# Kernel tuning notes

Measured on AMD Instinct MI355X. Metric: run time of the kernel, lower is better.

## Reference

```python
import jax, jax.numpy as jnp
import numpy as np

INF = 1e8
EPS = 1e-6
STRIDES = (8, 16, 32, 64, 128)
FEAT_SIZES = ((100, 128), (50, 64), (25, 32), (13, 16), (7, 8))
NUM_CLASSES = 81  # args.num_classes + 1
BG = NUM_CLASSES
TOPK1, TOPK2 = 3, 1
RATIO = 0.9
FRACTION = 0.5
B, G = 16, 32
NPER = [h * w for h, w in FEAT_SIZES]
OFFS = np.cumsum([0] + NPER)


def gen_trf():
    j = [2 ** i for i in range(8)]
    r1 = 1 + 6 * j[0]; r2 = r1 + 2 * j[1]
    p2 = r2 + 2 * j[2] * 3; r3 = p2 + 2 * j[2]
    p3 = r3 + 2 * j[3] * 3; r4 = p3 + 2 * j[3]
    p4 = r4 + 2 * j[4] * 5; r5 = p4 + 2 * j[4]
    p5 = r5 + 2 * j[5] * 2
    p6 = p5 + 2 * j[6]; p7 = p6 + 2 * j[7]
    return [p2, p3, p4, p5, p6, p7]


def make_points_rfields():
    trfs = gen_trf()
    pts, rfs = [], []
    for lvl, (h, w) in enumerate(FEAT_SIZES):
        s = STRIDES[lvl]
        xs = jnp.arange(w, dtype=jnp.float32) * s + s // 2
        ys = jnp.arange(h, dtype=jnp.float32) * s + s // 2
        Y, X = jnp.meshgrid(ys, xs, indexing='ij')
        p = jnp.stack([X.reshape(-1), Y.reshape(-1)], -1)
        pts.append(p)
        rf = trfs[lvl + 1] * FRACTION  # fpn_layer == 'p3' -> rfnum = lvl + 1
        rfs.append(jnp.concatenate([p - rf / 2, p + rf / 2], -1))
    return jnp.concatenate(pts, 0), jnp.concatenate(rfs, 0)


def kl_overlaps(gts, anc):
    # BboxDistanceMetric mode='kl': Gaussian KL divergence -> 1/(1+kl); (G, N)
    c1 = (gts[:, :2] + gts[:, 2:]) / 2
    c2 = (anc[:, :2] + anc[:, 2:]) / 2
    w1 = gts[:, 2] - gts[:, 0] + EPS; h1 = gts[:, 3] - gts[:, 1] + EPS
    w2 = anc[:, 2] - anc[:, 0] + EPS; h2 = anc[:, 3] - anc[:, 1] + EPS
    dx = c1[:, None, 0] - c2[None, :, 0]; dy = c1[:, None, 1] - c2[None, :, 1]
    w1s = (w1 ** 2)[:, None]; h1s = (h1 ** 2)[:, None]
    w2s = (w2 ** 2)[None, :]; h2s = (h2 ** 2)[None, :]
    kl = (w2s / w1s + h2s / h1s + 4 * dx ** 2 / w1s + 4 * dy ** 2 / h1s
          + jnp.log(w1s / w2s) + jnp.log(h1s / h2s) - 2) / 2
    return 1.0 / (1.0 + kl)


def hie_assign(rf1, rf2, gts):
    ov1 = kl_overlaps(gts, rf1)
    ov2 = kl_overlaps(gts, rf2)
    N = rf1.shape[0]; Gn = gts.shape[0]
    max_ov = ov1.max(0)
    assigned = jnp.where((max_ov >= 0) & (max_ov < 0.8), 0, -1).astype(jnp.int32)
    gt_ids = jnp.arange(1, Gn + 1, dtype=jnp.int32)
    _, i1 = jax.lax.top_k(ov1, TOPK1)  # (G, k1)
    s1 = jnp.full((N,), -1, jnp.int32).at[i1.reshape(-1)].max(jnp.repeat(gt_ids, TOPK1))
    assigned = jnp.where(s1 > 0, s1, assigned)
    _, i2 = jax.lax.top_k(ov2, TOPK2)  # (G, k2) second hierarchy overrides
    s2 = jnp.full((N,), -1, jnp.int32).at[i2.reshape(-1)].max(jnp.repeat(gt_ids, TOPK2))
    return jnp.where(s2 > 0, s2, assigned)


def target_single(gts, glabels, points, rf1, rf2):
    Gn = gts.shape[0]
    assigned = hie_assign(rf1, rf2, gts)  # (N,) 1-based gt index, 0/-1 = bg
    areas = (gts[:, 2] - gts[:, 0]) * (gts[:, 3] - gts[:, 1])
    mask = (assigned - 1)[:, None] == jnp.arange(Gn)[None, :]
    am = jnp.where(mask, areas[None, :], INF)
    min_area = am.min(1); mi = jnp.argmin(am, 1)
    lab = jnp.where(min_area >= INF, BG, glabels[mi])
    g = gts[mi]
    bt = jnp.stack([points[:, 0] - g[:, 0], points[:, 1] - g[:, 1],
                    g[:, 2] - points[:, 0], g[:, 3] - points[:, 1]], -1)
    return lab, bt


def diou_loss(pred, tgt):
    lt = jnp.maximum(pred[:, :2], tgt[:, :2])
    rb = jnp.minimum(pred[:, 2:], tgt[:, 2:])
    wh = jnp.clip(rb - lt, 0.0)
    ov = wh[:, 0] * wh[:, 1]
    ap = (pred[:, 2] - pred[:, 0]) * (pred[:, 3] - pred[:, 1])
    ag = (tgt[:, 2] - tgt[:, 0]) * (tgt[:, 3] - tgt[:, 1])
    ious = ov / (ap + ag - ov + EPS)
    elt = jnp.minimum(pred[:, :2], tgt[:, :2])
    erb = jnp.maximum(pred[:, 2:], tgt[:, 2:])
    ewh = jnp.clip(erb - elt, 0.0)
    c2 = ewh[:, 0] ** 2 + ewh[:, 1] ** 2 + EPS
    rho2 = ((pred[:, 0] + pred[:, 2] - tgt[:, 0] - tgt[:, 2]) ** 2
            + (pred[:, 1] + pred[:, 3] - tgt[:, 1] - tgt[:, 3]) ** 2) / 4
    return 1.0 - (ious - rho2 / c2)


def _forward(cls_l, bbox_l, ctr_l, gt_bboxes, gt_labels):
    points, rf1 = make_points_rfields()
    c = (rf1[:, :2] + rf1[:, 2:]) / 2
    wh = (rf1[:, 2:] - rf1[:, :2]) * RATIO
    rf2 = jnp.concatenate([c - wh / 2, c + wh / 2], -1)
    labels_all, targets_all = jax.vmap(target_single, (0, 0, None, None, None))(
        gt_bboxes, gt_labels, points, rf1, rf2)
    labels_all = jax.lax.stop_gradient(labels_all)
    targets_all = jax.lax.stop_gradient(targets_all)
    # flatten level-major, image-minor (matches torch.cat order in loss)
    fc = jnp.concatenate([t.transpose(0, 2, 3, 1).reshape(-1, NUM_CLASSES) for t in cls_l], 0)
    fb = jnp.concatenate([t.transpose(0, 2, 3, 1).reshape(-1, 4) for t in bbox_l], 0)
    fo = jnp.concatenate([t.transpose(0, 2, 3, 1).reshape(-1) for t in ctr_l], 0)
    fl = jnp.concatenate([labels_all[:, OFFS[i]:OFFS[i + 1]].reshape(-1) for i in range(5)], 0)
    ft = jnp.concatenate([targets_all[:, OFFS[i]:OFFS[i + 1]].reshape(-1, 4) for i in range(5)], 0)
    fp = jnp.concatenate([jnp.tile(points[OFFS[i]:OFFS[i + 1]], (B, 1)) for i in range(5)], 0)
    pos = fl < BG
    posf = pos.astype(fc.dtype)
    num_pos = jnp.maximum(posf.sum(), 1.0)
    # sigmoid focal loss (alpha=0.25, gamma=2); bg label -> all-zero one-hot
    tgt = jax.nn.one_hot(fl, NUM_CLASSES, dtype=fc.dtype)
    p = jax.nn.sigmoid(fc)
    pt = (1 - p) * tgt + p * (1 - tgt)
    fw = (0.25 * tgt + 0.75 * (1 - tgt)) * pt ** 2
    bce = jnp.maximum(fc, 0) - fc * tgt + jnp.log1p(jnp.exp(-jnp.abs(fc)))
    loss_cls = (bce * fw).sum() / num_pos
    # centerness target (sanitized on negatives to avoid nan)
    bt = jnp.where(pos[:, None], ft, 1.0)
    lr_min = jnp.minimum(bt[:, 0], bt[:, 2]); lr_max = jnp.maximum(bt[:, 0], bt[:, 2])
    tb_min = jnp.minimum(bt[:, 1], bt[:, 3]); tb_max = jnp.maximum(bt[:, 1], bt[:, 3])
    ctr_tgt = jnp.sqrt(jnp.clip((lr_min / lr_max) * (tb_min / tb_max), 0.0)) * posf
    denom = jnp.maximum(ctr_tgt.sum(), 1e-6)
    # decode distances to boxes and DIoU loss weighted by centerness
    x, y = fp[:, 0], fp[:, 1]
    pb = jnp.stack([x - fb[:, 0], y - fb[:, 1], x + fb[:, 2], y + fb[:, 3]], -1)
    tb_box = jnp.stack([x - bt[:, 0], y - bt[:, 1], x + bt[:, 2], y + bt[:, 3]], -1)
    loss_bbox = (diou_loss(pb, tb_box) * ctr_tgt).sum() / denom
    # centerness BCE-with-logits, averaged by num_pos
    bce_c = jnp.maximum(fo, 0) - fo * ctr_tgt + jnp.log1p(jnp.exp(-jnp.abs(fo)))
    loss_ctr = (bce_c * posf).sum() / num_pos
    return jnp.stack([loss_cls, loss_bbox, loss_ctr])


def setup_inputs() -> dict:
    key = jax.random.key(0)
    ks = jax.random.split(key, 24)
    cls_l = [jax.random.normal(ks[i], (B, NUM_CLASSES, h, w), jnp.float32) - 4.0
             for i, (h, w) in enumerate(FEAT_SIZES)]
    bbox_l = [jax.random.uniform(ks[5 + i], (B, 4, h, w), jnp.float32) * 64.0 + 1.0
              for i, (h, w) in enumerate(FEAT_SIZES)]
    ctr_l = [jax.random.normal(ks[10 + i], (B, 1, h, w), jnp.float32)
             for i, (h, w) in enumerate(FEAT_SIZES)]
    cx = jax.random.uniform(ks[15], (B, G)) * 1000.0 + 12.0
    cy = jax.random.uniform(ks[16], (B, G)) * 776.0 + 12.0
    w = jax.random.uniform(ks[17], (B, G)) * 240.0 + 8.0
    h = jax.random.uniform(ks[18], (B, G)) * 240.0 + 8.0
    gt_bboxes = jnp.stack([cx - w / 2, cy - h / 2, cx + w / 2, cy + h / 2], -1)
    gt_labels = jax.random.randint(ks[19], (B, G), 0, 80)
    d = {}
    for i in range(5):
        d[f'cls{i}'] = cls_l[i]; d[f'bbox{i}'] = bbox_l[i]; d[f'ctr{i}'] = ctr_l[i]
    d['gt_bboxes'] = gt_bboxes
    d['gt_labels'] = gt_labels
    return d


def reference(cls0, cls1, cls2, cls3, cls4, bbox0, bbox1, bbox2, bbox3, bbox4,
              ctr0, ctr1, ctr2, ctr3, ctr4, gt_bboxes, gt_labels):
    return _forward([cls0, cls1, cls2, cls3, cls4],
                    [bbox0, bbox1, bbox2, bbox3, bbox4],
                    [ctr0, ctr1, ctr2, ctr3, ctr4], gt_bboxes, gt_labels)
```

## Files before the change

### kernel.cpp

```cpp
#include <hip/hip_runtime.h>
#include <math.h>
#include <limits.h>

#pragma clang fp contract(off)

#define N_ANCH 17064
#define BATCH  16
#define NGT    32
#define EPSF   1e-6f

#define NPB     512
#define NSTREAM 2048
#define L2E 1.44269504088896340736f
#define LN2 0.69314718055994530942f

#define C1   4147200
#define C2   5184000
#define C3   5443200
#define C4   5510592
#define TOT4 5528736

#define CTR_IMG 0
#define CTR_SUB 16
#define CTR_GLB 32

__device__ __forceinline__ float fexp2(float x){ return __builtin_amdgcn_exp2f(x); }
__device__ __forceinline__ float flog2(float x){ return __builtin_amdgcn_logf(x); }
__device__ __forceinline__ float frcp (float x){ return __builtin_amdgcn_rcpf(x); }

__device__ __forceinline__ void astore_u32(unsigned int* p, unsigned int v) {
  __hip_atomic_store(p, v, __ATOMIC_RELAXED, __HIP_MEMORY_SCOPE_AGENT);
}
__device__ __forceinline__ unsigned int aload_u32(const unsigned int* p) {
  return __hip_atomic_load(p, __ATOMIC_RELAXED, __HIP_MEMORY_SCOPE_AGENT);
}
__device__ __forceinline__ void astore_u64(unsigned long long* p, unsigned long long v) {
  __hip_atomic_store(p, v, __ATOMIC_RELAXED, __HIP_MEMORY_SCOPE_AGENT);
}
__device__ __forceinline__ unsigned long long aload_u64(const unsigned long long* p) {
  return __hip_atomic_load(p, __ATOMIC_RELAXED, __HIP_MEMORY_SCOPE_AGENT);
}
#define VMCNT0() asm volatile("s_waitcnt vmcnt(0)" ::: "memory")

struct Geo { int lvl; int j; int HW; float px; float py; };

__device__ __forceinline__ Geo geom(int n) {
  Geo g;
  if (n < 12800)      { g.lvl=0; g.j=n;       g.HW=12800; g.px=(float)((g.j & 127)*8 + 4);   g.py=(float)((g.j >> 7)*8 + 4);   }
  else if (n < 16000) { g.lvl=1; g.j=n-12800; g.HW=3200;  g.px=(float)((g.j & 63)*16 + 8);   g.py=(float)((g.j >> 6)*16 + 8);  }
  else if (n < 16800) { g.lvl=2; g.j=n-16000; g.HW=800;   g.px=(float)((g.j & 31)*32 + 16);  g.py=(float)((g.j >> 5)*32 + 16); }
  else if (n < 17008) { g.lvl=3; g.j=n-16800; g.HW=208;   g.px=(float)((g.j & 15)*64 + 32);  g.py=(float)((g.j >> 4)*64 + 32); }
  else                { g.lvl=4; g.j=n-17008; g.HW=56;    g.px=(float)((g.j & 7)*128 + 64);  g.py=(float)((g.j >> 3)*128 + 64);}
  return g;
}

__device__ __forceinline__ bool bet(float av, int ai, float bv, int bi) {
  return (av < bv) || (av == bv && ai < bi);
}

__device__ __forceinline__ void insert3min(float* v, int* i, float nv, int ni) {
  if (nv < v[0])      { v[2]=v[1]; i[2]=i[1]; v[1]=v[0]; i[1]=i[0]; v[0]=nv; i[0]=ni; }
  else if (nv < v[1]) { v[2]=v[1]; i[2]=i[1]; v[1]=nv; i[1]=ni; }
  else                { v[2]=nv; i[2]=ni; }
}

__device__ __forceinline__ void insert3tie(float* v, int* i, float nv, int ni) {
  if (!bet(nv, ni, v[2], i[2])) return;
  if (bet(nv, ni, v[0], i[0]))      { v[2]=v[1]; i[2]=i[1]; v[1]=v[0]; i[1]=i[0]; v[0]=nv; i[0]=ni; }
  else if (bet(nv, ni, v[1], i[1])) { v[2]=v[1]; i[2]=i[1]; v[1]=nv; i[1]=ni; }
  else                              { v[2]=nv; i[2]=ni; }
}

__device__ __forceinline__ float negterm(float x) {
  float ax = fabsf(x);
  float e  = fexp2(ax * -L2E);
  float r  = frcp(1.0f + e);
  float p  = (x >= 0.0f) ? r : e * r;
  float sp = fmaxf(x, 0.0f) + flog2(1.0f + e) * LN2;
  return 0.75f * (p * p) * sp;
}

__global__ void zeroK(int* __restrict__ ctr) {
  int i = threadIdx.x;
  if (i < 33) ctr[i] = 0;
}

__device__ __forceinline__ void final_combine(const unsigned long long* __restrict__ bpart,
                                              const unsigned long long* __restrict__ gsum,
                                              float* __restrict__ out,
                                              double* R, int t) {
  if (t < 16) {
    R[t]      = __longlong_as_double(aload_u64(&gsum[t]));
    R[16+t]   = __longlong_as_double(aload_u64(&bpart[t*5+0]));
    R[32+t]   = __longlong_as_double(aload_u64(&bpart[t*5+1]));
    R[48+t]   = __longlong_as_double(aload_u64(&bpart[t*5+2]));
    R[64+t]   = __longlong_as_double(aload_u64(&bpart[t*5+3]));
    R[80+t]   = __longlong_as_double(aload_u64(&bpart[t*5+4]));
  }
  __syncthreads();
  if (t == 0) {
    double sc = 0.0, sp = 0.0, sct = 0.0, sdi = 0.0, scb = 0.0;
    for (int i = 0; i < 16; ++i) sc += R[i];
    for (int i = 0; i < 16; ++i) {
      sc  += R[16+i];
      sp  += R[32+i];
      sct += R[48+i];
      sdi += R[64+i];
      scb += R[80+i];
    }
    double np_ = sp > 1.0 ? sp : 1.0;
    double dn  = sct > 1e-6 ? sct : 1e-6;
    out[0] = (float)(sc / np_);
    out[1] = (float)(sdi / dn);
    out[2] = (float)(scb / np_);
  }
}

__global__ __launch_bounds__(256) void fusedK(
    const float4* __restrict__ gtb, const int* __restrict__ glab,
    const float* __restrict__ c0, const float* __restrict__ c1, const float* __restrict__ c2,
    const float* __restrict__ c3, const float* __restrict__ c4,
    const float* __restrict__ bb0, const float* __restrict__ bb1, const float* __restrict__ bb2,
    const float* __restrict__ bb3, const float* __restrict__ bb4,
    const float* __restrict__ ct0, const float* __restrict__ ct1, const float* __restrict__ ct2,
    const float* __restrict__ ct3, const float* __restrict__ ct4,
    unsigned int* __restrict__ win, unsigned int* __restrict__ part,
    unsigned long long* __restrict__ bpart, unsigned long long* __restrict__ gsum,
    int* __restrict__ ctr, float* __restrict__ out) {
  __shared__ float sv[768];
  __shared__ int   si[768];
  __shared__ float tv[256];
  __shared__ int   ti[256];
  __shared__ float sh[256];
  __shared__ unsigned int ukeys[128];
  __shared__ double r0[256], r1[256], r2[256], r3[256], r4[256];
  __shared__ int sflag, sflag2;

  int t  = threadIdx.x;
  int bi = blockIdx.x;

  if (bi >= NPB) {
    int sb = bi - NPB;
    float local = 0.0f;
    for (int i = sb * 256 + t; i < TOT4; i += NSTREAM * 256) {
      const float4* p; int off;
      if (i < C1)      { p = (const float4*)c0; off = i; }
      else if (i < C2) { p = (const float4*)c1; off = i - C1; }
      else if (i < C3) { p = (const float4*)c2; off = i - C2; }
      else if (i < C4) { p = (const float4*)c3; off = i - C3; }
      else             { p = (const float4*)c4; off = i - C4; }
      float4 f = p[off];
      local += negterm(f.x);
      local += negterm(f.y);
      local += negterm(f.z);
      local += negterm(f.w);
    }
    sh[t] = local;
    __syncthreads();
    #pragma unroll
    for (int off = 128; off > 0; off >>= 1) {
      if (t < off) sh[t] += sh[t + off];
      __syncthreads();
    }
    if (t == 0) {
      astore_u32(&part[sb], __float_as_uint(sh[0]));
      VMCNT0();
      int old = atomicAdd(&ctr[CTR_SUB + (sb & 15)], 1);
      sflag = (old == 127);
    }
    __syncthreads();
    if (!sflag) return;

    int g = sb & 15;
    double v = 0.0;
    if (t < 128) v = (double)__uint_as_float(aload_u32(&part[g + (t << 4)]));
    r0[t] = v;
    __syncthreads();
    #pragma unroll
    for (int off = 128; off > 0; off >>= 1) {
      if (t < off) r0[t] += r0[t + off];
      __syncthreads();
    }
    if (t == 0) {
      astore_u64(&gsum[g], (unsigned long long)__double_as_longlong(r0[0]));
      VMCNT0();
      int old2 = atomicAdd(&ctr[CTR_GLB], 1);
      sflag2 = (old2 == 31);
    }
    __syncthreads();
    if (sflag2) final_combine(bpart, gsum, out, r0, t);
    return;
  }

  int blk = bi;
  int b = blk >> 5, g = blk & 31;
  {
    float4 GB = gtb[b * NGT + g];
    float c1x = (GB.x + GB.z) * 0.5f, c1y = (GB.y + GB.w) * 0.5f;
    float w1 = GB.z - GB.x + EPSF, h1 = GB.w - GB.y + EPSF;
    float w1s = w1 * w1, h1s = h1 * h1;
    float iw = 1.0f / w1s, ih = 1.0f / h1s;
    float iws = iw + ih;
    float Lg = logf(w1s) + logf(h1s);
    float Ay = 4.0f * ih;
    float Axc = 4.0f * iw;

    float v1[3] = {INFINITY, INFINITY, INFINITY};
    int   i1[3] = {INT_MAX, INT_MAX, INT_MAX};
    float v2 = INFINITY; int i2 = INT_MAX;

    #define DO_LEVEL(BASE, LGW, H, STRIDE, RF) do {                             \
      const int W_ = 1 << (LGW);                                                \
      float w2a = (RF) + 1e-6f;          float w2sa = w2a * w2a;                \
      float w2b = (RF) * 0.9f + 1e-6f;   float w2sb = w2b * w2b;                \
      float K1 = w2sa * iws + Lg - 2.0f * logf(w2sa) - 2.0f;                    \
      float K2 = w2sb * iws + Lg - 2.0f * logf(w2sb) - 2.0f;                    \
      int col = t & (W_ - 1);                                                   \
      float px = (float)(col * (STRIDE) + (STRIDE) / 2);                        \
      float dx = c1x - px;                                                      \
      float kx1 = Axc * dx * dx + K1;                                           \
      float kx2 = Axc * dx * dx + K2;                                           \
      int rstep = 256 >> (LGW);                                                 \
      for (int row = t >> (LGW); row < (H); row += rstep) {                     \
        float py = (float)(row * (STRIDE) + (STRIDE) / 2);                      \
        float dy = c1y - py;                                                    \
        float dy2 = dy * dy;                                                    \
        float k1 = fmaf(Ay, dy2, kx1);                                          \
        float k2 = fmaf(Ay, dy2, kx2);                                          \
        int n = (BASE) + (row << (LGW)) + col;                                  \
        if (k1 < v1[2]) insert3min(v1, i1, k1, n);                              \
        if (k2 < v2) { v2 = k2; i2 = n; }                                       \
      }                                                                         \
    } while (0)

    DO_LEVEL(0,     7, 100,   8,  45.5f);
    DO_LEVEL(12800, 6,  50,  16, 133.5f);
    DO_LEVEL(16000, 5,  25,  32, 213.5f);
    DO_LEVEL(16800, 4,  13,  64, 277.5f);
    DO_LEVEL(17008, 3,   7, 128, 405.5f);
    #undef DO_LEVEL

    sv[t*3+0] = v1[0]; sv[t*3+1] = v1[1]; sv[t*3+2] = v1[2];
    si[t*3+0] = i1[0]; si[t*3+1] = i1[1]; si[t*3+2] = i1[2];
    tv[t] = v2; ti[t] = i2;
    __syncthreads();
    for (int off = 128; off > 0; off >>= 1) {
      if (t < off) {
        #pragma unroll
        for (int k = 0; k < 3; ++k)
          insert3tie(&sv[t * 3], &si[t * 3], sv[(t + off) * 3 + k], si[(t + off) * 3 + k]);
        if (bet(tv[t + off], ti[t + off], tv[t], ti[t])) { tv[t] = tv[t + off]; ti[t] = ti[t + off]; }
      }
      __syncthreads();
    }
    if (t == 0) {
      astore_u32(&win[blk * 4 + 0], (unsigned int)si[0]);
      astore_u32(&win[blk * 4 + 1], (unsigned int)si[1]);
      astore_u32(&win[blk * 4 + 2], (unsigned int)si[2]);
      astore_u32(&win[blk * 4 + 3], (unsigned int)ti[0]);
      VMCNT0();
      int old = atomicAdd(&ctr[CTR_IMG + b], 1);
      sflag = (old == 31);
    }
    __syncthreads();
  }
  if (!sflag) return;

  if (t < 128) {
    int gg = t >> 2, s = t & 3;
    unsigned int n = aload_u32(&win[b * 128 + gg * 4 + s]);
    unsigned int pri = ((s == 3) ? 32u : 0u) + (unsigned int)gg;
    ukeys[t] = (n << 6) | pri;
  }
  __syncthreads();

  double a_cls = 0.0, a_pos = 0.0, a_ctr = 0.0, a_diou = 0.0, a_cbce = 0.0;

  if (t < 128) {
    unsigned int me = ukeys[t];
    unsigned int nn = me >> 6;
    bool alive = true;
    #pragma unroll 8
    for (int j = 0; j < 128; ++j) {
      unsigned int o = ukeys[j];
      if ((o >> 6) == nn && o > me) alive = false;
    }
    if (alive) {
      int n = (int)nn;
      int gg = (int)(me & 31u);
      int lab = glab[b * NGT + gg];
      float4 gb = gtb[b * NGT + gg];
      Geo G = geom(n);

      const float* bb; const float* ct; const float* cp;
      if (G.lvl == 0)      { bb = bb0; ct = ct0; cp = c0; }
      else if (G.lvl == 1) { bb = bb1; ct = ct1; cp = c1; }
      else if (G.lvl == 2) { bb = bb2; ct = ct2; cp = c2; }
      else if (G.lvl == 3) { bb = bb3; ct = ct3; cp = c3; }
      else                 { bb = bb4; ct = ct4; cp = c4; }

      const float* bp = bb + b * 4 * G.HW + G.j;
      float f0 = bp[0];
      float f1 = bp[G.HW];
      float f2 = bp[2 * G.HW];
      float f3 = bp[3 * G.HW];
      float fo = ct[b * G.HW + G.j];
      float xc = cp[((size_t)(b * 81 + lab)) * G.HW + G.j];

      {
        float ax = fabsf(xc);
        float e  = fexp2(ax * -L2E);
        float r  = frcp(1.0f + e);
        float p  = (xc >= 0.0f) ? r : e * r;
        float sp = fmaxf(xc, 0.0f) + flog2(1.0f + e) * LN2;
        float neg = 0.75f * (p * p) * sp;
        float omp = 1.0f - p;
        float pos = 0.25f * (omp * omp) * (sp - xc);
        a_cls += (double)(pos - neg);
      }

      float tx = G.px - gb.x, ty = G.py - gb.y, tz = gb.z - G.px, tw = gb.w - G.py;

      float lr_min = fminf(tx, tz), lr_max = fmaxf(tx, tz);
      float tb_min = fminf(ty, tw), tb_max = fmaxf(ty, tw);
      float prod = (lr_min / lr_max) * (tb_min / tb_max);
      float ctrt = sqrtf(fmaxf(prod, 0.0f));

      float pb0 = G.px - f0, pb1 = G.py - f1, pb2 = G.px + f2, pb3 = G.py + f3;
      float tb0 = G.px - tx, tb1 = G.py - ty, tb2 = G.px + tz, tb3 = G.py + tw;

      float ltx = fmaxf(pb0, tb0), lty = fmaxf(pb1, tb1);
      float rbx = fminf(pb2, tb2), rby = fminf(pb3, tb3);
      float whx = fmaxf(rbx - ltx, 0.0f), why = fmaxf(rby - lty, 0.0f);
      float ovl = whx * why;
      float ap = (pb2 - pb0) * (pb3 - pb1);
      float ag = (tb2 - tb0) * (tb3 - tb1);
      float ious = ovl / (ap + ag - ovl + EPSF);
      float eltx = fminf(pb0, tb0), elty = fminf(pb1, tb1);
      float erbx = fmaxf(pb2, tb2), erby = fmaxf(pb3, tb3);
      float ewx = fmaxf(erbx - eltx, 0.0f), ewy = fmaxf(erby - elty, 0.0f);
      float c2v = ewx * ewx + ewy * ewy + EPSF;
      float sx = pb0 + pb2 - tb0 - tb2;
      float sy = pb1 + pb3 - tb1 - tb3;
      float rho2 = (sx * sx + sy * sy) * 0.25f;
      float dl = 1.0f - (ious - rho2 / c2v);

      a_pos  += 1.0;
      a_ctr  += (double)ctrt;
      a_diou += (double)(dl * ctrt);
      a_cbce += (double)(fmaxf(fo, 0.0f) - fo * ctrt + log1pf(expf(-fabsf(fo))));
    }
  }

  r0[t] = a_cls; r1[t] = a_pos; r2[t] = a_ctr; r3[t] = a_diou; r4[t] = a_cbce;
  __syncthreads();
  #pragma unroll
  for (int off = 128; off > 0; off >>= 1) {
    if (t < off) {
      r0[t] += r0[t + off]; r1[t] += r1[t + off]; r2[t] += r2[t + off];
      r3[t] += r3[t + off]; r4[t] += r4[t + off];
    }
    __syncthreads();
  }

  if (t == 0) {
    astore_u64(&bpart[b * 5 + 0], (unsigned long long)__double_as_longlong(r0[0]));
    astore_u64(&bpart[b * 5 + 1], (unsigned long long)__double_as_longlong(r1[0]));
    astore_u64(&bpart[b * 5 + 2], (unsigned long long)__double_as_longlong(r2[0]));
    astore_u64(&bpart[b * 5 + 3], (unsigned long long)__double_as_longlong(r3[0]));
    astore_u64(&bpart[b * 5 + 4], (unsigned long long)__double_as_longlong(r4[0]));
    VMCNT0();
    int old2 = atomicAdd(&ctr[CTR_GLB], 1);
    sflag2 = (old2 == 31);
  }
  __syncthreads();
  if (sflag2) final_combine(bpart, gsum, out, r0, t);
}

extern "C" void kernel_launch(void* const* d_in, const int* in_sizes, int n_in,
                              void* d_out, int out_size, void* d_ws, size_t ws_size,
                              hipStream_t stream) {
  (void)in_sizes; (void)n_in; (void)out_size; (void)ws_size;
  const float* cls[5] = {(const float*)d_in[0],  (const float*)d_in[3],  (const float*)d_in[6],
                         (const float*)d_in[9],  (const float*)d_in[12]};
  const float* bbx[5] = {(const float*)d_in[1],  (const float*)d_in[4],  (const float*)d_in[7],
                         (const float*)d_in[10], (const float*)d_in[13]};
  const float* ctr_[5] = {(const float*)d_in[2],  (const float*)d_in[5],  (const float*)d_in[8],
                          (const float*)d_in[11], (const float*)d_in[14]};
  const float4* gtb = (const float4*)d_in[15];
  const int* glab = (const int*)d_in[16];

  char* ws = (char*)d_ws;
  unsigned int*       win   = (unsigned int*)ws;
  unsigned int*       part  = (unsigned int*)(ws + 8192);
  unsigned long long* bpart = (unsigned long long*)(ws + 16384);
  unsigned long long* gsum  = (unsigned long long*)(ws + 17024);
  int*                cnts  = (int*)(ws + 17152);

  zeroK<<<1, 64, 0, stream>>>(cnts);
  fusedK<<<NPB + NSTREAM, 256, 0, stream>>>(
      gtb, glab,
      cls[0], cls[1], cls[2], cls[3], cls[4],
      bbx[0], bbx[1], bbx[2], bbx[3], bbx[4],
      ctr_[0], ctr_[1], ctr_[2], ctr_[3], ctr_[4],
      win, part, bpart, gsum, cnts, (float*)d_out);
}
```

Measured before the change: 48.15 us.

## Reorder blocks, split streaming per level, unroll loads, and alias shared memory

Streaming blocks now come first in the grid and each is assigned to a single classification level with a fixed stride, which removes the per-element level branch. The loads are unrolled four deep to raise memory-level parallelism. All shared arrays are aliased into one 8.7KB buffer to cut LDS use and allow more blocks per CU. Reductions over 128 entries now start at offset 64, dropping a redundant step. The risks are uneven work across blocks assigned to different levels, and the assignment-heavy blocks now being scheduled last, which may lengthen the tail.

```diff
diff --git a/kernel.cpp b/kernel.cpp
--- a/kernel.cpp
+++ b/kernel.cpp
@@ -9,15 +9,11 @@
 #define NGT    32
 #define EPSF   1e-6f
 
+#define NSTREAM 2048
 #define NPB     512
-#define NSTREAM 2048
 #define L2E 1.44269504088896340736f
 #define LN2 0.69314718055994530942f
 
-#define C1   4147200
-#define C2   5184000
-#define C3   5443200
-#define C4   5510592
 #define TOT4 5528736
 
 #define CTR_IMG 0
@@ -127,34 +123,39 @@
     unsigned int* __restrict__ win, unsigned int* __restrict__ part,
     unsigned long long* __restrict__ bpart, unsigned long long* __restrict__ gsum,
     int* __restrict__ ctr, float* __restrict__ out) {
-  __shared__ float sv[768];
-  __shared__ int   si[768];
-  __shared__ float tv[256];
-  __shared__ int   ti[256];
-  __shared__ float sh[256];
-  __shared__ unsigned int ukeys[128];
-  __shared__ double r0[256], r1[256], r2[256], r3[256], r4[256];
+  __shared__ char smem[8704];
   __shared__ int sflag, sflag2;
 
   int t  = threadIdx.x;
   int bi = blockIdx.x;
 
-  if (bi >= NPB) {
-    int sb = bi - NPB;
+  if (bi < NSTREAM) {
+    const float4* p; int cnt, stride, sb0;
+    if (bi < 1536)      { p = (const float4*)c0; cnt = 4147200; stride = 393216; sb0 = bi; }
+    else if (bi < 1920) { p = (const float4*)c1; cnt = 1036800; stride = 98304;  sb0 = bi - 1536; }
+    else if (bi < 2016) { p = (const float4*)c2; cnt = 259200;  stride = 24576;  sb0 = bi - 1920; }
+    else if (bi < 2041) { p = (const float4*)c3; cnt = 67392;   stride = 6400;   sb0 = bi - 2016; }
+    else                { p = (const float4*)c4; cnt = 18144;   stride = 1792;   sb0 = bi - 2041; }
+
     float local = 0.0f;
-    for (int i = sb * 256 + t; i < TOT4; i += NSTREAM * 256) {
-      const float4* p; int off;
-      if (i < C1)      { p = (const float4*)c0; off = i; }
-      else if (i < C2) { p = (const float4*)c1; off = i - C1; }
-      else if (i < C3) { p = (const float4*)c2; off = i - C2; }
-      else if (i < C4) { p = (const float4*)c3; off = i - C3; }
-      else             { p = (const float4*)c4; off = i - C4; }
-      float4 f = p[off];
-      local += negterm(f.x);
-      local += negterm(f.y);
-      local += negterm(f.z);
-      local += negterm(f.w);
-    }
+    int i = sb0 * 256 + t;
+    for (; i + 3 * stride < cnt; i += 4 * stride) {
+      float4 A = p[i];
+      float4 B = p[i + stride];
+      float4 Cc = p[i + 2 * stride];
+      float4 D = p[i + 3 * stride];
+      local += negterm(A.x);  local += negterm(A.y);  local += negterm(A.z);  local += negterm(A.w);
+      local += negterm(B.x);  local += negterm(B.y);  local += negterm(B.z);  local += negterm(B.w);
+      local += negterm(Cc.x); local += negterm(Cc.y); local += negterm(Cc.z); local += negterm(Cc.w);
+      local += negterm(D.x);  local += negterm(D.y);  local += negterm(D.z);  local += negterm(D.w);
+    }
+    for (; i < cnt; i += stride) {
+      float4 f = p[i];
+      local += negterm(f.x); local += negterm(f.y); local += negterm(f.z); local += negterm(f.w);
+    }
+
+    float*  sh = (float*)smem;
+    double* rr = (double*)(smem + 1024);
     sh[t] = local;
     __syncthreads();
     #pragma unroll
@@ -163,38 +164,41 @@
       __syncthreads();
     }
     if (t == 0) {
-      astore_u32(&part[sb], __float_as_uint(sh[0]));
+      astore_u32(&part[bi], __float_as_uint(sh[0]));
       VMCNT0();
-      int old = atomicAdd(&ctr[CTR_SUB + (sb & 15)], 1);
+      int old = atomicAdd(&ctr[CTR_SUB + (bi & 15)], 1);
       sflag = (old == 127);
     }
     __syncthreads();
     if (!sflag) return;
 
-    int g = sb & 15;
-    double v = 0.0;
-    if (t < 128) v = (double)__uint_as_float(aload_u32(&part[g + (t << 4)]));
-    r0[t] = v;
+    int g = bi & 15;
+    if (t < 128) rr[t] = (double)__uint_as_float(aload_u32(&part[g + (t << 4)]));
     __syncthreads();
     #pragma unroll
-    for (int off = 128; off > 0; off >>= 1) {
-      if (t < off) r0[t] += r0[t + off];
+    for (int off = 64; off > 0; off >>= 1) {
+      if (t < off) rr[t] += rr[t + off];
       __syncthreads();
     }
     if (t == 0) {
-      astore_u64(&gsum[g], (unsigned long long)__double_as_longlong(r0[0]));
+      astore_u64(&gsum[g], (unsigned long long)__double_as_longlong(rr[0]));
       VMCNT0();
       int old2 = atomicAdd(&ctr[CTR_GLB], 1);
       sflag2 = (old2 == 31);
     }
     __syncthreads();
-    if (sflag2) final_combine(bpart, gsum, out, r0, t);
+    if (sflag2) final_combine(bpart, gsum, out, rr, t);
     return;
   }
 
-  int blk = bi;
+  int blk = bi - NSTREAM;
   int b = blk >> 5, g = blk & 31;
   {
+    float* sv = (float*)smem;
+    int*   si = (int*)(smem + 3072);
+    float* tv = (float*)(smem + 6144);
+    int*   ti = (int*)(smem + 7168);
+
     float4 GB = gtb[b * NGT + g];
     float c1x = (GB.x + GB.z) * 0.5f, c1y = (GB.y + GB.w) * 0.5f;
     float w1 = GB.z - GB.x + EPSF, h1 = GB.w - GB.y + EPSF;
@@ -266,6 +270,13 @@
   }
   if (!sflag) return;
 
+  unsigned int* ukeys = (unsigned int*)smem;
+  double* r0 = (double*)(smem + 512);
+  double* r1 = (double*)(smem + 1536);
+  double* r2 = (double*)(smem + 2560);
+  double* r3 = (double*)(smem + 3584);
+  double* r4 = (double*)(smem + 4608);
+
   if (t < 128) {
     int gg = t >> 2, s = t & 3;
     unsigned int n = aload_u32(&win[b * 128 + gg * 4 + s]);
@@ -352,10 +363,10 @@
     }
   }
 
-  r0[t] = a_cls; r1[t] = a_pos; r2[t] = a_ctr; r3[t] = a_diou; r4[t] = a_cbce;
+  if (t < 128) { r0[t] = a_cls; r1[t] = a_pos; r2[t] = a_ctr; r3[t] = a_diou; r4[t] = a_cbce; }
   __syncthreads();
   #pragma unroll
-  for (int off = 128; off > 0; off >>= 1) {
+  for (int off = 64; off > 0; off >>= 1) {
     if (t < off) {
       r0[t] += r0[t + off]; r1[t] += r1[t + off]; r2[t] += r2[t + off];
       r3[t] += r3[t + off]; r4[t] += r4[t + off];
@@ -398,7 +409,7 @@
   int*                cnts  = (int*)(ws + 17152);
 
   zeroK<<<1, 64, 0, stream>>>(cnts);
-  fusedK<<<NPB + NSTREAM, 256, 0, stream>>>(
+  fusedK<<<NSTREAM + NPB, 256, 0, stream>>>(
       gtb, glab,
       cls[0], cls[1], cls[2], cls[3], cls[4],
       bbx[0], bbx[1], bbx[2], bbx[3], bbx[4],
```

New measurement: 52.41 us. 1.09x slower.
